# Kernel optimization log

Measured on AMD Instinct MI355X. Metric: run time of the kernel, lower is better.

## Reference

```python
import jax, jax.numpy as jnp
from jax import lax
import numpy as np

TAU = 10.0      # tauSr == tauRef
THR = 1.0       # theta
WIDTH = 1.0     # tauRho (surrogate width)
SCALE = 1.0     # scaleRho (surrogate scale)
DECAY = float(np.exp(-1.0 / TAU))


@jax.custom_vjp
def _heaviside(v):
    # spike = 1[v >= theta]
    return (v >= THR).astype(v.dtype)

def _heaviside_fwd(v):
    return _heaviside(v), v

def _heaviside_bwd(v, g):
    # SLAYER exponential surrogate pdf: scaleRho/tauRho * exp(-|v-theta|/tauRho)
    return (g * (SCALE / WIDTH) * jnp.exp(-jnp.abs(v - THR) / WIDTH),)

_heaviside.defvjp(_heaviside_fwd, _heaviside_bwd)


def _conv2d(x, w, pad):
    # x: (B, Cin, H, W), w: (Cout, Cin, kh, kw); SLAYER convs have no bias
    return lax.conv_general_dilated(
        x, w, window_strides=(1, 1), padding=[(pad, pad), (pad, pad)],
        dimension_numbers=("NCHW", "OIHW", "NCHW"))


def _sumpool(x, k):
    # SLAYER pool = sum over kxk window (times a learned scalar applied outside)
    B, C, H, W = x.shape
    return x.reshape(B, C, H // k, k, W // k, k).sum(axis=(3, 5))


def _psp(seq):
    # exponential synaptic (PSP) filter along time: s[t] = a*s[t-1] + x[t]
    a = jnp.asarray(DECAY, seq.dtype)
    def step(s, x_t):
        s = a * s + x_t
        return s, s
    _, out = lax.scan(step, jnp.zeros_like(seq[0]), seq)
    return out  # (T, ...)


def _spikes(u):
    # thresholded spiking with decaying refractory feedback (scaleRef=1):
    # v[t] = u[t] - r[t]; s[t] = 1[v >= theta]; r[t+1] = b*(r[t] + theta*s[t])
    b = jnp.asarray(DECAY, u.dtype)
    def step(r, u_t):
        s = _heaviside(u_t - r)
        r_next = b * (r + THR * s)
        return r_next, s
    _, out = lax.scan(step, jnp.zeros_like(u[0]), u)
    return out  # (T, ...)


def _forward(x, conv1_w, conv2_w, lin_w, w_pool1, w_pool2):
    N, T, C, H, W = x.shape  # (64, 100, 2, 32, 32)
    h = _conv2d(x.reshape(N * T, C, H, W), conv1_w, 2)        # (NT, 4, 32, 32)
    h = _sumpool(h, 4) * w_pool1                               # (NT, 4, 8, 8)
    h = h.reshape(N, T, 4, 8, 8).swapaxes(0, 1)                # (T, N, 4, 8, 8)
    s1 = _spikes(_psp(h))                                      # (T, N, 4, 8, 8)
    h2 = _conv2d(s1.reshape(T * N, 4, 8, 8), conv2_w, 1)       # (TN, 8, 8, 8)
    h2 = (_sumpool(h2, 2) * w_pool2).reshape(T, N, 8, 4, 4)    # (T, N, 8, 4, 4)
    s2 = _spikes(_psp(h2))                                     # (T, N, 8, 4, 4)
    # dense = full-spatial conv (2, 8, 4, 4) -> (N, T, 2)
    return jnp.einsum("tnchw,ochw->nto", s2, lin_w)


def setup_inputs() -> dict:
    key = jax.random.key(0)
    ks = jax.random.split(key, 4)
    x = (jax.random.uniform(ks[0], (64, 100, 2, 32, 32)) < 0.1).astype(jnp.float32)
    conv1_w = jax.random.normal(ks[1], (4, 2, 5, 5), jnp.float32) * 0.3
    conv2_w = jax.random.normal(ks[2], (8, 4, 3, 3), jnp.float32) * 0.3
    lin_w = jax.random.normal(ks[3], (2, 8, 4, 4), jnp.float32) * 0.3
    w_pool1 = jnp.float32(1.0 / 16.0)  # 1.1*theta / (16 * 1.1)
    w_pool2 = jnp.float32(1.0 / 4.0)   # 1.1*theta / (4 * 1.1)
    return {"x": x, "conv1_w": conv1_w, "conv2_w": conv2_w, "lin_w": lin_w,
            "w_pool1": w_pool1, "w_pool2": w_pool2}


def reference(x, conv1_w, conv2_w, lin_w, w_pool1, w_pool2):
    return _forward(x, conv1_w, conv2_w, lin_w, w_pool1, w_pool2)
```

## Files before the change

### kernel.cpp

```cpp
#include <hip/hip_runtime.h>


#define DECAY 0.9048374180359595f

#define BAR_LGKM() asm volatile("s_waitcnt lgkmcnt(0)\n\ts_barrier" ::: "memory")
#define FENCE_LGKM() asm volatile("s_waitcnt lgkmcnt(0)" ::: "memory")

__global__ __launch_bounds__(128) void k0_fold(const float* __restrict__ w1,
        const float* __restrict__ w2, const float* __restrict__ wp1,
        const float* __restrict__ wp2, float* __restrict__ wl1,
        float* __restrict__ wl2, float* __restrict__ out) {
    const int tid = threadIdx.x;
    out[blockIdx.x * 128 + tid] = 0.f;
    if (blockIdx.x != 0) return;
    const float p1 = wp1[0], p2 = wp2[0];
    for (int idx = tid; idx < 512; idx += 128) {
        const int f = idx & 7, c = (idx >> 3) & 3, e = (idx >> 5) & 7, cin = idx >> 8;
        const int cc = c * 2 + cin;
        int alo = e - 3; if (alo < 0) alo = 0;
        int ahi = e;     if (ahi > 4) ahi = 4;
        int blo = f - 3; if (blo < 0) blo = 0;
        int bhi = f;     if (bhi > 4) bhi = 4;
        float s = 0.f;
        for (int a = alo; a <= ahi; ++a)
            for (int b = blo; b <= bhi; ++b)
                s += w1[cc * 25 + a * 5 + b];
        wl1[(cin * 8 + e) * 32 + c * 8 + f] = s * p1;
    }
    for (int idx = tid; idx < 512; idx += 128) {
        const int c2 = idx & 7, f = (idx >> 3) & 3, e = (idx >> 5) & 3, cin = idx >> 7;
        int alo = e - 1; if (alo < 0) alo = 0;
        int ahi = e;     if (ahi > 2) ahi = 2;
        int blo = f - 1; if (blo < 0) blo = 0;
        int bhi = f;     if (bhi > 2) bhi = 2;
        float s = 0.f;
        for (int aa = alo; aa <= ahi; ++aa)
            for (int bb = blo; bb <= bhi; ++bb)
                s += w2[((c2 * 4 + cin) * 3 + aa) * 3 + bb];
        wl2[c2 * 68 + cin * 16 + e * 4 + f] = s * p2;
    }
}

__global__ __launch_bounds__(64) void k1(const float* __restrict__ x,
        const float* __restrict__ wg, float* __restrict__ u1) {
    __shared__ __align__(16) float xs[2 * 1296];
    __shared__ __align__(16) float wl[512];
    const int lane = threadIdx.x;
    const int frame = blockIdx.x;
    const int n = frame / 100, t = frame % 100;

    *(float4*)(wl + 4 * lane)       = *(const float4*)(wg + 4 * lane);
    *(float4*)(wl + 256 + 4 * lane) = *(const float4*)(wg + 256 + 4 * lane);

    #pragma unroll
    for (int m0 = 0; m0 < 128; m0 += 64) {
        const int m = m0 + lane;
        if (m < 72) {
            const int cin = m / 36, rem = m % 36;
            const int rr = rem / 9, q4 = rem % 9;
            const int pr = (rr == 0) ? 0 : (rr == 1) ? 9 : (rr == 2) ? 26 : 35;
            *(float4*)(xs + cin * 1296 + pr * 36 + q4 * 4) = make_float4(0.f, 0.f, 0.f, 0.f);
        }
    }
    #pragma unroll
    for (int m0 = 0; m0 < 192; m0 += 64) {
        const int m = m0 + lane;
        if (m < 144) {
            const int cin = m / 72, rem = m % 72;
            const int side = rem & 1, pr = rem >> 1;
            *(float2*)(xs + cin * 1296 + pr * 36 + side * 34) = make_float2(0.f, 0.f);
        }
    }
    const float4* xg = (const float4*)(x + (size_t)frame * 2048);
    #pragma unroll
    for (int q = 0; q < 8; ++q) {
        const int m = q * 64 + lane;
        const float4 v = xg[m];
        const int li = 4 * m;
        const int cin = li >> 10, row = (li >> 5) & 31, col = li & 31;
        const int r = row + 2;
        const int pr = (r & 3) * 9 + (r >> 2);
        float* d = xs + cin * 1296 + pr * 36 + col + 2;
        *(float2*)(d)     = make_float2(v.x, v.y);
        *(float2*)(d + 2) = make_float2(v.z, v.w);
    }
    FENCE_LGKM();

    const int cp = lane >> 5;
    const int i  = (lane >> 2) & 7;
    const int jh = (lane >> 1) & 1;
    const int eh = lane & 1;

    float acc[2][4] = {{0.f, 0.f, 0.f, 0.f}, {0.f, 0.f, 0.f, 0.f}};
    const float* tb = xs + (i + eh) * 36 + jh * 16;
    #pragma unroll
    for (int cin = 0; cin < 2; ++cin) {
        #pragma unroll
        for (int et = 0; et < 4; ++et) {
            const int ro = cin * 1296 + et * 9 * 36;
            float xr[20];
            #pragma unroll
            for (int b = 0; b < 5; ++b)
                *(float4*)(xr + 4 * b) = *(const float4*)(tb + ro + 4 * b);
            float wv[16];
            const float* wp = wl + (cin * 8 + eh * 4 + et) * 32 + cp * 16;
            #pragma unroll
            for (int q = 0; q < 4; ++q)
                *(float4*)(wv + 4 * q) = *(const float4*)(wp + 4 * q);
            #pragma unroll
            for (int cl = 0; cl < 2; ++cl) {
                #pragma unroll
                for (int jj = 0; jj < 4; ++jj) {
                    const int o = 4 * jj;
                    acc[cl][jj] += xr[o]*wv[cl*8]     + xr[o+1]*wv[cl*8+1]
                                 + xr[o+2]*wv[cl*8+2] + xr[o+3]*wv[cl*8+3]
                                 + xr[o+4]*wv[cl*8+4] + xr[o+5]*wv[cl*8+5]
                                 + xr[o+6]*wv[cl*8+6] + xr[o+7]*wv[cl*8+7];
                }
            }
        }
    }
    #pragma unroll
    for (int cl = 0; cl < 2; ++cl)
        #pragma unroll
        for (int jj = 0; jj < 4; ++jj)
            acc[cl][jj] += __shfl_xor(acc[cl][jj], 1);

    const float o0 = eh ? acc[1][0] : acc[0][0];
    const float o1 = eh ? acc[1][1] : acc[0][1];
    const float o2 = eh ? acc[1][2] : acc[0][2];
    const float o3 = eh ? acc[1][3] : acc[0][3];
    *(float4*)(u1 + (size_t)t * 16384 + n * 256 + (2 * cp + eh) * 64 + i * 8 + jh * 4) =
        make_float4(o0, o1, o2, o3);
}

__global__ __launch_bounds__(256) void kf(const float* __restrict__ u1,
        const float* __restrict__ wl2g, const float* __restrict__ lw,
        float* __restrict__ out) {
    __shared__ __align__(16) float ls1[100 * 260];
    __shared__ __align__(16) float ls2[100 * 36];
    const int tid = threadIdx.x;
    const int n = blockIdx.x >> 2, qtr = blockIdx.x & 3;
    const int wave = tid >> 6, l64 = tid & 63;
    const float a = DECAY;

    const float* up = u1 + n * 256 + tid;

    const int sub = tid >> 4, l16 = tid & 15;
    const int c2l = l16 >> 3, i2 = (l16 >> 1) & 3, jhp = l16 & 1;
    const int c2g = qtr * 2 + c2l;

    float4 wreg[16];
    {
        const float* wbase = wl2g + c2g * 68;
        #pragma unroll
        for (int q = 0; q < 16; ++q)
            wreg[q] = *(const float4*)(wbase + (q >> 2) * 16 + (q & 3) * 4);
    }

    float dwA[8], dwB[8];
    {
        const int idx = l64 & 3;
        #pragma unroll
        for (int m = 0; m < 8; ++m) {
            dwA[m] = lw[qtr * 32 + idx * 8 + m];
            dwB[m] = lw[128 + qtr * 32 + idx * 8 + m];
        }
    }

    float vbuf[100];
    #pragma unroll
    for (int k = 0; k < 100; ++k) vbuf[k] = up[(size_t)k * 16384];
    {
        float psp = 0.f, rr = 0.f;
        #pragma unroll
        for (int k = 0; k < 100; ++k) {
            psp = a * psp + vbuf[k];
            const float vv = psp - rr;
            const float s = (vv >= 1.f) ? 1.f : 0.f;
            rr = a * (rr + s);
            ls1[k * 260 + tid] = s;
        }
    }
    BAR_LGKM();

    #pragma unroll 1
    for (int pass = 0; pass < 7; ++pass) {
        const int slot = sub + 16 * pass;
        if (slot < 100) {
            const float* sb = ls1 + slot * 260;
            float acc0 = 0.f, acc1 = 0.f;
            #pragma unroll
            for (int cin = 0; cin < 4; ++cin) {
                #pragma unroll
                for (int e = 0; e < 4; ++e) {
                    const int ri = 2 * i2 + e - 1;
                    const int rc = (ri < 0) ? 0 : (ri > 7 ? 7 : ri);
                    const bool rok = (ri >= 0) && (ri <= 7);
                    float rr8[8];
                    const float* rp = sb + cin * 64 + rc * 8;
                    *(float4*)(rr8)     = *(const float4*)(rp);
                    *(float4*)(rr8 + 4) = *(const float4*)(rp + 4);
                    float xr[6];
                    xr[0] = jhp ? rr8[3] : 0.0f;
                    xr[1] = jhp ? rr8[4] : rr8[0];
                    xr[2] = jhp ? rr8[5] : rr8[1];
                    xr[3] = jhp ? rr8[6] : rr8[2];
                    xr[4] = jhp ? rr8[7] : rr8[3];
                    xr[5] = jhp ? 0.0f   : rr8[4];
                    if (!rok) {
                        #pragma unroll
                        for (int m = 0; m < 6; ++m) xr[m] = 0.0f;
                    }
                    const float4 wf = wreg[cin * 4 + e];
                    acc0 += xr[0] * wf.x; acc0 += xr[1] * wf.y;
                    acc0 += xr[2] * wf.z; acc0 += xr[3] * wf.w;
                    acc1 += xr[2] * wf.x; acc1 += xr[3] * wf.y;
                    acc1 += xr[4] * wf.z; acc1 += xr[5] * wf.w;
                }
            }
            *(float2*)(ls2 + slot * 36 + c2l * 16 + i2 * 4 + 2 * jhp) =
                make_float2(acc0, acc1);
        }
    }
    BAR_LGKM();

    if (wave == 0) {
        if (l64 < 32) {
            float psp2 = 0.f, rr2 = 0.f;
            #pragma unroll
            for (int k = 0; k < 100; ++k) {
                const float u = ls2[k * 36 + l64];
                psp2 = a * psp2 + u;
                const float vv = psp2 - rr2;
                const float s = (vv >= 1.f) ? 1.f : 0.f;
                rr2 = a * (rr2 + s);
                ls2[k * 36 + l64] = s;
            }
        }
        FENCE_LGKM();
        const int idx = l64 & 3;
        #pragma unroll 1
        for (int pass = 0; pass < 7; ++pass) {
            const int slot = (l64 >> 2) + 16 * pass;
            if (slot < 100) {
                float a0 = 0.f, a1 = 0.f;
                #pragma unroll
                for (int m = 0; m < 8; ++m) {
                    const float s = ls2[slot * 36 + idx * 8 + m];
                    a0 += s * dwA[m];
                    a1 += s * dwB[m];
                }
                a0 += __shfl_down(a0, 2); a0 += __shfl_down(a0, 1);
                a1 += __shfl_down(a1, 2); a1 += __shfl_down(a1, 1);
                if (idx == 0) {
                    atomicAdd(&out[n * 200 + slot * 2],     a0);
                    atomicAdd(&out[n * 200 + slot * 2 + 1], a1);
                }
            }
        }
    }
}

extern "C" void kernel_launch(void* const* d_in, const int* in_sizes, int n_in,
                              void* d_out, int out_size, void* d_ws, size_t ws_size,
                              hipStream_t stream) {
    const float* x   = (const float*)d_in[0];
    const float* w1  = (const float*)d_in[1];
    const float* w2  = (const float*)d_in[2];
    const float* lw  = (const float*)d_in[3];
    const float* wp1 = (const float*)d_in[4];
    const float* wp2 = (const float*)d_in[5];

    float* u1  = (float*)d_ws;
    float* wl1 = u1 + 1638400;
    float* wl2 = wl1 + 512;
    float* out = (float*)d_out;

    k0_fold<<<100, 128, 0, stream>>>(w1, w2, wp1, wp2, wl1, wl2, out);
    k1<<<6400, 64, 0, stream>>>(x, wl1, u1);
    kf<<<256, 256, 0, stream>>>(u1, wl2, lw, out);
}
```

Baseline: 121.0 us.

## Fuse layer-2 spiking scan with dense readout and remap block-to-sample order

The dense readout is now computed inside the second spiking scan. Each of 32 lanes holds its own weight, and a wave-level xor-shuffle reduction plus atomicAdd runs at each time step, but only when some lane spiked (checked with a ballot). This removes the separate pass that wrote spikes back to shared memory and reread them. The ls2 inputs are preloaded into registers first. Block indices are also remapped so neighbouring blocks handle different samples and quarters, which changes the atomic contention and cache pattern. In exchange, the serial scan now carries shuffle reductions and atomics on its critical path, and register pressure rises from the 100-entry buffer.

```diff
diff --git a/kernel.cpp b/kernel.cpp
--- a/kernel.cpp
+++ b/kernel.cpp
@@ -140,7 +140,9 @@
     __shared__ __align__(16) float ls1[100 * 260];
     __shared__ __align__(16) float ls2[100 * 36];
     const int tid = threadIdx.x;
-    const int n = blockIdx.x >> 2, qtr = blockIdx.x & 3;
+    const int bid = blockIdx.x;
+    const int n = (bid & 7) * 8 + (bid >> 5);
+    const int qtr = (bid >> 3) & 3;
     const int wave = tid >> 6, l64 = tid & 63;
     const float a = DECAY;
 
@@ -158,15 +160,9 @@
             wreg[q] = *(const float4*)(wbase + (q >> 2) * 16 + (q & 3) * 4);
     }
 
-    float dwA[8], dwB[8];
-    {
-        const int idx = l64 & 3;
-        #pragma unroll
-        for (int m = 0; m < 8; ++m) {
-            dwA[m] = lw[qtr * 32 + idx * 8 + m];
-            dwB[m] = lw[128 + qtr * 32 + idx * 8 + m];
-        }
-    }
+    const int cell = l64 & 31;
+    const float w0 = lw[qtr * 32 + cell];
+    const float w1 = lw[128 + qtr * 32 + cell];
 
     float vbuf[100];
     #pragma unroll
@@ -225,37 +221,28 @@
     }
     BAR_LGKM();
 
-    if (wave == 0) {
-        if (l64 < 32) {
-            float psp2 = 0.f, rr2 = 0.f;
-            #pragma unroll
-            for (int k = 0; k < 100; ++k) {
-                const float u = ls2[k * 36 + l64];
-                psp2 = a * psp2 + u;
-                const float vv = psp2 - rr2;
-                const float s = (vv >= 1.f) ? 1.f : 0.f;
-                rr2 = a * (rr2 + s);
-                ls2[k * 36 + l64] = s;
-            }
-        }
-        FENCE_LGKM();
-        const int idx = l64 & 3;
-        #pragma unroll 1
-        for (int pass = 0; pass < 7; ++pass) {
-            const int slot = (l64 >> 2) + 16 * pass;
-            if (slot < 100) {
-                float a0 = 0.f, a1 = 0.f;
+    if (wave == 0 && l64 < 32) {
+        float ub[100];
+        #pragma unroll
+        for (int k = 0; k < 100; ++k) ub[k] = ls2[k * 36 + l64];
+        float psp2 = 0.f, rr2 = 0.f;
+        #pragma unroll
+        for (int k = 0; k < 100; ++k) {
+            psp2 = a * psp2 + ub[k];
+            const float vv = psp2 - rr2;
+            const float s = (vv >= 1.f) ? 1.f : 0.f;
+            rr2 = a * (rr2 + s);
+            const unsigned long long b = __ballot(s != 0.f);
+            if (b) {
+                float p0 = s * w0, p1 = s * w1;
                 #pragma unroll
-                for (int m = 0; m < 8; ++m) {
-                    const float s = ls2[slot * 36 + idx * 8 + m];
-                    a0 += s * dwA[m];
-                    a1 += s * dwB[m];
-                }
-                a0 += __shfl_down(a0, 2); a0 += __shfl_down(a0, 1);
-                a1 += __shfl_down(a1, 2); a1 += __shfl_down(a1, 1);
-                if (idx == 0) {
-                    atomicAdd(&out[n * 200 + slot * 2],     a0);
-                    atomicAdd(&out[n * 200 + slot * 2 + 1], a1);
+                for (int m = 16; m >= 1; m >>= 1) {
+                    p0 += __shfl_xor(p0, m);
+                    p1 += __shfl_xor(p1, m);
+                }
+                if (l64 == 0) {
+                    atomicAdd(&out[n * 200 + k * 2],     p0);
+                    atomicAdd(&out[n * 200 + k * 2 + 1], p1);
                 }
             }
         }
```

After: 125.8 us. 1.04x slower.
